# Kernel optimization log

Measured on AMD Instinct MI355X. Metric: run time of the kernel, lower is better.

## Reference

```python
import jax, jax.numpy as jnp
import numpy as np
import math

B, T, D = 2, 2048, 1024
H, HKV = 16, 4
HD = D // H            # 64
G = H // HKV           # GQA group size = 4
ROPE_BASE = 10000.0


def _rope(x, cos, sin):
    # x: [B, T, h, HD]; rotate-half rotary embedding
    half = x.shape[-1] // 2
    x1, x2 = x[..., :half], x[..., half:]
    c = cos[None, :, None, :]  # [1,T,1,HD/2]
    s = sin[None, :, None, :]
    return jnp.concatenate([x1 * c - x2 * s, x1 * s + x2 * c], axis=-1)


def setup_inputs() -> dict:
    key = jax.random.key(0)
    ks = jax.random.split(key, 6)
    sD = 1.0 / math.sqrt(D)
    x = jax.random.normal(ks[0], (B, T, D), dtype=jnp.float32)
    Wq = jax.random.normal(ks[1], (D, D), dtype=jnp.float32) * sD
    Wk = jax.random.normal(ks[2], (HKV * HD, D), dtype=jnp.float32) * sD
    Wv = jax.random.normal(ks[3], (HKV * HD, D), dtype=jnp.float32) * sD
    Wp = jax.random.normal(ks[4], (D, D), dtype=jnp.float32) * sD
    q_gain = jnp.full((H,), 0.125, dtype=jnp.float32)  # qk_gain_init
    return {"x": x, "Wq": Wq, "Wk": Wk, "Wv": Wv, "Wp": Wp, "q_gain": q_gain}


def reference(x, Wq, Wk, Wv, Wp, q_gain):
    Bx, Tx, _ = x.shape
    # QKV projections (CastedLinear == plain no-bias linear in fp32 here)
    q = (x @ Wq.T).reshape(Bx, Tx, H, HD)
    k = (x @ Wk.T).reshape(Bx, Tx, HKV, HD)
    v = (x @ Wv.T).reshape(Bx, Tx, HKV, HD)

    # rotary tables
    inv_freq = 1.0 / (ROPE_BASE ** (jnp.arange(0, HD, 2, dtype=jnp.float32) / HD))
    freqs = jnp.arange(Tx, dtype=jnp.float32)[:, None] * inv_freq[None, :]  # [T, HD/2]
    cos, sin = jnp.cos(freqs), jnp.sin(freqs)

    q = _rope(q, cos, sin) * q_gain[None, None, :, None]  # per-head learned gain
    k = _rope(k, cos, sin)

    # grouped-query causal attention
    qg = q.reshape(Bx, Tx, HKV, G, HD)
    scale = 1.0 / math.sqrt(HD)
    scores = jnp.einsum('bqkgd,bskd->bkgqs', qg, k) * scale  # [B,HKV,G,T,T]
    causal = jnp.tril(jnp.ones((Tx, Tx), dtype=bool))
    scores = jnp.where(causal[None, None, None], scores, jnp.float32(-1e30))
    p = jax.nn.softmax(scores, axis=-1)
    o = jnp.einsum('bkgqs,bskd->bqkgd', p, v).reshape(Bx, Tx, D)
    return o @ Wp.T
```

## Files before the change

### kernel.cpp

```cpp
#include <hip/hip_runtime.h>

typedef unsigned short u16;
typedef unsigned int   u32;
typedef __bf16 bfv8 __attribute__((ext_vector_type(8)));
typedef float  f32x4 __attribute__((ext_vector_type(4)));
typedef short  s16x4 __attribute__((ext_vector_type(4)));

#define B_   2
#define T_   2048
#define D_   1024
#define H_   16
#define HKV_ 4
#define NQK  1280
#define BT_  (B_*T_)
#define QSCALE 0.18033688011112042f
#define L2_10K 0.41524101186092515f
#define I2PI   0.15915494309189535f

__device__ __forceinline__ u16 f2bf(float f) {
  __bf16 h = (__bf16)f; u16 s; __builtin_memcpy(&s, &h, 2); return s;
}

__device__ __forceinline__ void load16(const u16* g, u16* l) {
  auto gp = (const __attribute__((address_space(1))) u32*)(uintptr_t)g;
  auto lp = (__attribute__((address_space(3))) u32*)(uintptr_t)l;
  __builtin_amdgcn_global_load_lds(gp, lp, 16, 0, 0);
}

__device__ __forceinline__ void hw_sincos_rev(float rev, float& s, float& c) {
  rev -= floorf(rev);
  s = __builtin_amdgcn_sinf(rev);
  c = __builtin_amdgcn_cosf(rev);
}

__global__ void conv_kernel(const float* __restrict__ src, u16* __restrict__ dst, int n) {
  int i = (blockIdx.x * 256 + threadIdx.x) * 4;
  if (i >= n) return;
  float4 v = *(const float4*)(src + i);
  ushort4 o; o.x = f2bf(v.x); o.y = f2bf(v.y); o.z = f2bf(v.z); o.w = f2bf(v.w);
  *(ushort4*)(dst + i) = o;
}
__global__ void conv_w_kernel(const float* __restrict__ wq, const float* __restrict__ wk,
                              const float* __restrict__ wv, const float* __restrict__ wp,
                              u16* __restrict__ dst) {
  int i = (blockIdx.x * 256 + threadIdx.x) * 4;
  const float* s; int off;
  if      (i < 1048576) { s = wq; off = i; }
  else if (i < 1310720) { s = wk; off = i - 1048576; }
  else if (i < 1572864) { s = wv; off = i - 1310720; }
  else                  { s = wp; off = i - 1572864; }
  float4 v = *(const float4*)(s + off);
  ushort4 o; o.x = f2bf(v.x); o.y = f2bf(v.y); o.z = f2bf(v.z); o.w = f2bf(v.w);
  *(ushort4*)(dst + i) = o;
}

template<int MODE>
__global__ __launch_bounds__(256) void gemm_bt(const u16* __restrict__ A,
                                               const u16* __restrict__ Bm,
                                               void* __restrict__ C,
                                               u16* __restrict__ vT,
                                               const float* __restrict__ qg,
                                               int M, int N, int K) {
  __shared__ __align__(16) u16 As[128 * 32];
  __shared__ __align__(16) u16 Bs[128 * 32];
  const int tid  = threadIdx.x;
  const int wave = tid >> 6, lane = tid & 63;
  const int quad = lane >> 4, l16 = lane & 15;
  const int m0 = blockIdx.y * 128, n0 = blockIdx.x * 128;
  const int wm = (wave >> 1) * 64, wn = (wave & 1) * 64;
  const int lr = lane >> 2, lc = (lane & 3) * 8;

  f32x4 acc[4][4];
  for (int mi = 0; mi < 4; ++mi)
    for (int ni = 0; ni < 4; ++ni) acc[mi][ni] = (f32x4){0.f, 0.f, 0.f, 0.f};

  for (int kk = 0; kk < K; kk += 32) {
    __syncthreads();
    #pragma unroll
    for (int u = 0; u < 2; ++u) {
      const int c = wave * 2 + u;
      const int r = c * 16 + lr;
      load16(A  + (size_t)(m0 + r) * K + kk + lc, As + c * 512);
      load16(Bm + (size_t)(n0 + r) * K + kk + lc, Bs + c * 512);
    }
    __syncthreads();
    bfv8 af[4], bf_[4];
    #pragma unroll
    for (int i = 0; i < 4; ++i) af[i]  = *(const bfv8*)(As + (wm + i*16 + l16)*32 + 8*quad);
    #pragma unroll
    for (int i = 0; i < 4; ++i) bf_[i] = *(const bfv8*)(Bs + (wn + i*16 + l16)*32 + 8*quad);
    #pragma unroll
    for (int mi = 0; mi < 4; ++mi)
      #pragma unroll
      for (int ni = 0; ni < 4; ++ni)
        acc[mi][ni] = __builtin_amdgcn_mfma_f32_16x16x32_bf16(af[mi], bf_[ni], acc[mi][ni], 0, 0, 0);
  }

  if (MODE == 0) {
    #pragma unroll
    for (int mi = 0; mi < 4; ++mi)
      #pragma unroll
      for (int ni = 0; ni < 4; ++ni)
        #pragma unroll
        for (int r = 0; r < 4; ++r)
          ((float*)C)[(size_t)(m0 + wm + mi*16 + 4*quad + r) * N + n0 + wn + ni*16 + l16]
            = acc[mi][ni][r];
  } else {
    const int colbase = n0 + wn;
    if (colbase < NQK) {
      const bool isQ = colbase < 1024;
      const float gain = isQ ? qg[colbase >> 6] * QSCALE : 1.0f;
      const float inv0 = exp2f(-(float)l16 * L2_10K) * I2PI;
      const float inv1 = exp2f(-(float)(l16 + 16) * L2_10K) * I2PI;
      #pragma unroll
      for (int mi = 0; mi < 4; ++mi) {
        const int rowg = m0 + wm + mi*16 + 4*quad;
        u16* dst = (u16*)C + (size_t)rowg * NQK + colbase + l16;
        #pragma unroll
        for (int r = 0; r < 4; ++r) {
          const int t = (rowg + r) & (T_ - 1);
          float s0, c0, s1, c1;
          hw_sincos_rev((float)t * inv0, s0, c0);
          hw_sincos_rev((float)t * inv1, s1, c1);
          const float x1a = acc[mi][0][r], x2a = acc[mi][2][r];
          const float x1b = acc[mi][1][r], x2b = acc[mi][3][r];
          u16* drow = dst + (size_t)r * NQK;
          drow[0]  = f2bf((x1a*c0 - x2a*s0) * gain);
          drow[16] = f2bf((x1b*c1 - x2b*s1) * gain);
          drow[32] = f2bf((x1a*s0 + x2a*c0) * gain);
          drow[48] = f2bf((x1b*s1 + x2b*c1) * gain);
        }
      }
    } else {
      #pragma unroll
      for (int mi = 0; mi < 4; ++mi)
        #pragma unroll
        for (int ni = 0; ni < 4; ++ni) {
          const int dd  = colbase + ni*16 + l16 - NQK;
          const int kvh = dd >> 6, d = dd & 63;
          const int rowg = m0 + wm + mi*16 + 4*quad;
          const int bb = rowg >> 11, t = rowg & (T_ - 1);
          ushort4 w4;
          w4.x = f2bf(acc[mi][ni][0]); w4.y = f2bf(acc[mi][ni][1]);
          w4.z = f2bf(acc[mi][ni][2]); w4.w = f2bf(acc[mi][ni][3]);
          *(ushort4*)(vT + ((size_t)((bb*HKV_ + kvh)*64 + d)) * T_ + t) = w4;
        }
    }
  }
}

template<bool DOA, bool DIAGA, bool DIAGB>
__device__ __forceinline__ void attn_tile(const u16* KB, const u16* VB,
                                          int l16, int quad,
                                          const bfv8* qA, const bfv8* qB,
                                          float& psA, float& psB,
                                          f32x4 oA[4], f32x4 oB[4],
                                          int qColA, int qColB, int s0) {
  const int sw = l16 & 7;
  f32x4 stA[4], stB[4];
  #pragma unroll
  for (int ni = 0; ni < 4; ++ni) {
    const int row = ni*16 + l16;
    bfv8 k0 = *(const bfv8*)(KB + row*64 + 8*(quad ^ sw));
    bfv8 k1 = *(const bfv8*)(KB + row*64 + 8*((quad + 4) ^ sw));
    if (DOA) {
      stA[ni] = __builtin_amdgcn_mfma_f32_16x16x32_bf16(k0, qA[0], (f32x4){0.f,0.f,0.f,0.f}, 0, 0, 0);
      stA[ni] = __builtin_amdgcn_mfma_f32_16x16x32_bf16(k1, qA[1], stA[ni], 0, 0, 0);
    }
    stB[ni] = __builtin_amdgcn_mfma_f32_16x16x32_bf16(k0, qB[0], (f32x4){0.f,0.f,0.f,0.f}, 0, 0, 0);
    stB[ni] = __builtin_amdgcn_mfma_f32_16x16x32_bf16(k1, qB[1], stB[ni], 0, 0, 0);
  }
  s16x4 pbA[4], pbB[4];
  #pragma unroll
  for (int ni = 0; ni < 4; ++ni)
    #pragma unroll
    for (int r = 0; r < 4; ++r) {
      const int key = s0 + ni*16 + 4*quad + r;
      if (DOA) {
        float v = stA[ni][r];
        if (DIAGA) v = (key <= qColA) ? v : -3.0e38f;
        const float p = __builtin_amdgcn_exp2f(v);
        psA += p;
        pbA[ni][r] = (short)f2bf(p);
      }
      float v = stB[ni][r];
      if (DIAGB) v = (key <= qColB) ? v : -3.0e38f;
      const float p = __builtin_amdgcn_exp2f(v);
      psB += p;
      pbB[ni][r] = (short)f2bf(p);
    }
  #pragma unroll
  for (int ni = 0; ni < 4; ++ni) {
    const int vofs = 8*((2*ni + (quad >> 1)) ^ sw) + 4*(quad & 1);
    #pragma unroll
    for (int dt = 0; dt < 4; ++dt) {
      s16x4 va = *(const s16x4*)(VB + (dt*16 + l16)*64 + vofs);
      if (DOA) oA[dt] = __builtin_amdgcn_mfma_f32_16x16x16bf16_1k(va, pbA[ni], oA[dt], 0, 0, 0);
      oB[dt] = __builtin_amdgcn_mfma_f32_16x16x16bf16_1k(va, pbB[ni], oB[dt], 0, 0, 0);
    }
  }
}

__global__ __launch_bounds__(256) void attn_kernel(const u16* __restrict__ qkv,
                                                   const u16* __restrict__ vT,
                                                   u16* __restrict__ o) {
  const int pr = blockIdx.x;
  const int h  = blockIdx.y;
  const int b  = blockIdx.z;
  const int kvh = h >> 2;
  const int tid = threadIdx.x;
  const int wave = tid >> 6, lane = tid & 63;
  const int quad = lane >> 4, l16 = lane & 15;

  const int qtA = pr, qtB = 31 - pr;
  const int nk  = qtB + 1;

  __shared__ __align__(16) u16 Kl[2][64 * 64];
  __shared__ __align__(16) u16 Vl[2][64 * 64];

  const u16* qAp = qkv + (size_t)(b*T_ + qtA*64 + wave*16 + l16) * NQK + h*64 + 8*quad;
  const u16* qBp = qkv + (size_t)(b*T_ + qtB*64 + wave*16 + l16) * NQK + h*64 + 8*quad;
  const bfv8 qA[2] = { *(const bfv8*)qAp, *(const bfv8*)(qAp + 32) };
  const bfv8 qB[2] = { *(const bfv8*)qBp, *(const bfv8*)(qBp + 32) };

  float psA = 0.f, psB = 0.f;
  f32x4 oA[4], oB[4];
  #pragma unroll
  for (int d = 0; d < 4; ++d) oA[d] = oB[d] = (f32x4){0.f, 0.f, 0.f, 0.f};

  const int srow = lane >> 3, slot = lane & 7;
  const u16* Kg = qkv + (size_t)(b*T_) * NQK + 1024 + kvh*64;
  const u16* Vg = vT  + (size_t)((b*HKV_ + kvh) * 64) * T_;

  auto stage = [&](int kt, int buf) {
    const int s0 = kt * 64;
    #pragma unroll
    for (int u = 0; u < 2; ++u) {
      const int base = wave*16 + u*8;
      const int r  = base + srow;
      const int kc = slot ^ (r & 7);
      load16(Kg + (size_t)(s0 + r) * NQK + kc*8, Kl[buf] + base*64);
      load16(Vg + (size_t)r * T_ + s0 + kc*8,    Vl[buf] + base*64);
    }
  };

  stage(0, 0);
  const int qColA = qtA*64 + wave*16 + l16;
  const int qColB = qtB*64 + wave*16 + l16;

  for (int kt = 0; kt < qtA; ++kt) {
    __syncthreads();
    stage(kt + 1, (kt + 1) & 1);
    attn_tile<true, false, false>(Kl[kt & 1], Vl[kt & 1], l16, quad, qA, qB,
                                  psA, psB, oA, oB, qColA, qColB, kt*64);
  }
  {
    const int kt = qtA;
    __syncthreads();
    stage(kt + 1, (kt + 1) & 1);
    attn_tile<true, true, false>(Kl[kt & 1], Vl[kt & 1], l16, quad, qA, qB,
                                 psA, psB, oA, oB, qColA, qColB, kt*64);
  }
  for (int kt = qtA + 1; kt < nk - 1; ++kt) {
    __syncthreads();
    stage(kt + 1, (kt + 1) & 1);
    attn_tile<false, false, false>(Kl[kt & 1], Vl[kt & 1], l16, quad, qA, qB,
                                   psA, psB, oA, oB, qColA, qColB, kt*64);
  }
  {
    const int kt = nk - 1;
    __syncthreads();
    attn_tile<false, false, true>(Kl[kt & 1], Vl[kt & 1], l16, quad, qA, qB,
                                  psA, psB, oA, oB, qColA, qColB, kt*64);
  }

  #pragma unroll
  for (int off = 16; off < 64; off <<= 1) {
    psA += __shfl_xor(psA, off);
    psB += __shfl_xor(psB, off);
  }
  const float ivA = 1.0f / psA, ivB = 1.0f / psB;

  #pragma unroll
  for (int dt = 0; dt < 4; ++dt) {
    ushort4 wA, wB;
    wA.x = f2bf(oA[dt][0]*ivA); wA.y = f2bf(oA[dt][1]*ivA);
    wA.z = f2bf(oA[dt][2]*ivA); wA.w = f2bf(oA[dt][3]*ivA);
    wB.x = f2bf(oB[dt][0]*ivB); wB.y = f2bf(oB[dt][1]*ivB);
    wB.z = f2bf(oB[dt][2]*ivB); wB.w = f2bf(oB[dt][3]*ivB);
    *(ushort4*)(o + (size_t)(b*T_ + qColA) * D_ + h*64 + dt*16 + 4*quad) = wA;
    *(ushort4*)(o + (size_t)(b*T_ + qColB) * D_ + h*64 + dt*16 + 4*quad) = wB;
  }
}

extern "C" void kernel_launch(void* const* d_in, const int* in_sizes, int n_in,
                              void* d_out, int out_size, void* d_ws, size_t ws_size,
                              hipStream_t stream) {
  const float* x  = (const float*)d_in[0];
  const float* Wq = (const float*)d_in[1];
  const float* Wk = (const float*)d_in[2];
  const float* Wv = (const float*)d_in[3];
  const float* Wp = (const float*)d_in[4];
  const float* qg = (const float*)d_in[5];

  u16* xb   = (u16*)d_ws;
  u16* wqkv = xb   + (size_t)BT_ * D_;
  u16* wpb  = wqkv + (size_t)1536 * D_;
  u16* qkvb = wpb  + (size_t)D_ * D_;
  u16* vT   = qkvb + (size_t)BT_ * NQK;
  u16* ob   = xb;

  conv_kernel<<<dim3((BT_*D_/4 + 255)/256), dim3(256), 0, stream>>>(x, xb, BT_*D_);
  conv_w_kernel<<<dim3(2560), dim3(256), 0, stream>>>(Wq, Wk, Wv, Wp, wqkv);

  gemm_bt<2><<<dim3(12, 32), dim3(256), 0, stream>>>(xb, wqkv, qkvb, vT, qg, BT_, 1536, D_);
  attn_kernel<<<dim3(16, H_, B_), dim3(256), 0, stream>>>(qkvb, vT, ob);
  gemm_bt<0><<<dim3(8, 32), dim3(256), 0, stream>>>(ob, wpb, d_out, (u16*)nullptr, nullptr, BT_, D_, D_);
}
```

Measured before the change: 174.5 us.

## Fuse input conversions into one kernel and shrink GEMM tiles to 128x64

The separate x and weight fp32-to-bf16 conversion kernels are merged into one launch, which relies on xb and wqkv being contiguous in the workspace. The GEMM block tile changes from 128x128 with four waves to 128x64 with two waves, doubling the grid for both projections so small GEMMs occupy more of the GPU's compute units. Each wave still computes a 64x64 subtile, but B-tile reuse across waves is lower and A tiles are loaded twice as often overall.

```diff
diff --git a/kernel.cpp b/kernel.cpp
--- a/kernel.cpp
+++ b/kernel.cpp
@@ -33,41 +33,39 @@
   c = __builtin_amdgcn_cosf(rev);
 }
 
-__global__ void conv_kernel(const float* __restrict__ src, u16* __restrict__ dst, int n) {
-  int i = (blockIdx.x * 256 + threadIdx.x) * 4;
-  if (i >= n) return;
-  float4 v = *(const float4*)(src + i);
-  ushort4 o; o.x = f2bf(v.x); o.y = f2bf(v.y); o.z = f2bf(v.z); o.w = f2bf(v.w);
-  *(ushort4*)(dst + i) = o;
-}
-__global__ void conv_w_kernel(const float* __restrict__ wq, const float* __restrict__ wk,
-                              const float* __restrict__ wv, const float* __restrict__ wp,
-                              u16* __restrict__ dst) {
+__global__ void conv_all_kernel(const float* __restrict__ x,
+                                const float* __restrict__ wq, const float* __restrict__ wk,
+                                const float* __restrict__ wv, const float* __restrict__ wp,
+                                u16* __restrict__ dst) {
   int i = (blockIdx.x * 256 + threadIdx.x) * 4;
   const float* s; int off;
-  if      (i < 1048576) { s = wq; off = i; }
-  else if (i < 1310720) { s = wk; off = i - 1048576; }
-  else if (i < 1572864) { s = wv; off = i - 1310720; }
-  else                  { s = wp; off = i - 1572864; }
+  if (i < 4194304) { s = x; off = i; }
+  else {
+    int j = i - 4194304;
+    if      (j < 1048576) { s = wq; off = j; }
+    else if (j < 1310720) { s = wk; off = j - 1048576; }
+    else if (j < 1572864) { s = wv; off = j - 1310720; }
+    else                  { s = wp; off = j - 1572864; }
+  }
   float4 v = *(const float4*)(s + off);
   ushort4 o; o.x = f2bf(v.x); o.y = f2bf(v.y); o.z = f2bf(v.z); o.w = f2bf(v.w);
   *(ushort4*)(dst + i) = o;
 }
 
 template<int MODE>
-__global__ __launch_bounds__(256) void gemm_bt(const u16* __restrict__ A,
+__global__ __launch_bounds__(128) void gemm_bt(const u16* __restrict__ A,
                                                const u16* __restrict__ Bm,
                                                void* __restrict__ C,
                                                u16* __restrict__ vT,
                                                const float* __restrict__ qg,
                                                int M, int N, int K) {
   __shared__ __align__(16) u16 As[128 * 32];
-  __shared__ __align__(16) u16 Bs[128 * 32];
+  __shared__ __align__(16) u16 Bs[64 * 32];
   const int tid  = threadIdx.x;
   const int wave = tid >> 6, lane = tid & 63;
   const int quad = lane >> 4, l16 = lane & 15;
-  const int m0 = blockIdx.y * 128, n0 = blockIdx.x * 128;
-  const int wm = (wave >> 1) * 64, wn = (wave & 1) * 64;
+  const int m0 = blockIdx.y * 128, n0 = blockIdx.x * 64;
+  const int wm = wave * 64;
   const int lr = lane >> 2, lc = (lane & 3) * 8;
 
   f32x4 acc[4][4];
@@ -77,18 +75,21 @@
   for (int kk = 0; kk < K; kk += 32) {
     __syncthreads();
     #pragma unroll
+    for (int u = 0; u < 4; ++u) {
+      const int c = u * 2 + wave;
+      load16(A + (size_t)(m0 + c*16 + lr) * K + kk + lc, As + c * 512);
+    }
+    #pragma unroll
     for (int u = 0; u < 2; ++u) {
-      const int c = wave * 2 + u;
-      const int r = c * 16 + lr;
-      load16(A  + (size_t)(m0 + r) * K + kk + lc, As + c * 512);
-      load16(Bm + (size_t)(n0 + r) * K + kk + lc, Bs + c * 512);
+      const int c = u * 2 + wave;
+      load16(Bm + (size_t)(n0 + c*16 + lr) * K + kk + lc, Bs + c * 512);
     }
     __syncthreads();
     bfv8 af[4], bf_[4];
     #pragma unroll
     for (int i = 0; i < 4; ++i) af[i]  = *(const bfv8*)(As + (wm + i*16 + l16)*32 + 8*quad);
     #pragma unroll
-    for (int i = 0; i < 4; ++i) bf_[i] = *(const bfv8*)(Bs + (wn + i*16 + l16)*32 + 8*quad);
+    for (int i = 0; i < 4; ++i) bf_[i] = *(const bfv8*)(Bs + (i*16 + l16)*32 + 8*quad);
     #pragma unroll
     for (int mi = 0; mi < 4; ++mi)
       #pragma unroll
@@ -103,19 +104,18 @@
       for (int ni = 0; ni < 4; ++ni)
         #pragma unroll
         for (int r = 0; r < 4; ++r)
-          ((float*)C)[(size_t)(m0 + wm + mi*16 + 4*quad + r) * N + n0 + wn + ni*16 + l16]
+          ((float*)C)[(size_t)(m0 + wm + mi*16 + 4*quad + r) * N + n0 + ni*16 + l16]
             = acc[mi][ni][r];
   } else {
-    const int colbase = n0 + wn;
-    if (colbase < NQK) {
-      const bool isQ = colbase < 1024;
-      const float gain = isQ ? qg[colbase >> 6] * QSCALE : 1.0f;
+    if (n0 < NQK) {
+      const bool isQ = n0 < 1024;
+      const float gain = isQ ? qg[n0 >> 6] * QSCALE : 1.0f;
       const float inv0 = exp2f(-(float)l16 * L2_10K) * I2PI;
       const float inv1 = exp2f(-(float)(l16 + 16) * L2_10K) * I2PI;
       #pragma unroll
       for (int mi = 0; mi < 4; ++mi) {
         const int rowg = m0 + wm + mi*16 + 4*quad;
-        u16* dst = (u16*)C + (size_t)rowg * NQK + colbase + l16;
+        u16* dst = (u16*)C + (size_t)rowg * NQK + n0 + l16;
         #pragma unroll
         for (int r = 0; r < 4; ++r) {
           const int t = (rowg + r) & (T_ - 1);
@@ -132,12 +132,12 @@
         }
       }
     } else {
+      const int kvh = (n0 - NQK) >> 6;
       #pragma unroll
       for (int mi = 0; mi < 4; ++mi)
         #pragma unroll
         for (int ni = 0; ni < 4; ++ni) {
-          const int dd  = colbase + ni*16 + l16 - NQK;
-          const int kvh = dd >> 6, d = dd & 63;
+          const int d = ni*16 + l16;
           const int rowg = m0 + wm + mi*16 + 4*quad;
           const int bb = rowg >> 11, t = rowg & (T_ - 1);
           ushort4 w4;
@@ -310,10 +310,10 @@
   u16* vT   = qkvb + (size_t)BT_ * NQK;
   u16* ob   = xb;
 
-  conv_kernel<<<dim3((BT_*D_/4 + 255)/256), dim3(256), 0, stream>>>(x, xb, BT_*D_);
-  conv_w_kernel<<<dim3(2560), dim3(256), 0, stream>>>(Wq, Wk, Wv, Wp, wqkv);
-
-  gemm_bt<2><<<dim3(12, 32), dim3(256), 0, stream>>>(xb, wqkv, qkvb, vT, qg, BT_, 1536, D_);
+  conv_all_kernel<<<dim3((4194304 + 2621440) / 1024), dim3(256), 0, stream>>>(
+      x, Wq, Wk, Wv, Wp, xb);
+
+  gemm_bt<2><<<dim3(24, 32), dim3(128), 0, stream>>>(xb, wqkv, qkvb, vT, qg, BT_, 1536, D_);
   attn_kernel<<<dim3(16, H_, B_), dim3(256), 0, stream>>>(qkvb, vT, ob);
-  gemm_bt<0><<<dim3(8, 32), dim3(256), 0, stream>>>(ob, wpb, d_out, (u16*)nullptr, nullptr, BT_, D_, D_);
-}
+  gemm_bt<0><<<dim3(16, 32), dim3(128), 0, stream>>>(ob, wpb, d_out, (u16*)nullptr, nullptr, BT_, D_, D_);
+}
```

Measured after the change: 174.3 us. About the same (-0.1%).
